# Kernel optimization log

Measured on AMD Instinct MI355X. Metric: run time of the kernel, lower is better.

## Reference

```python
import jax, jax.numpy as jnp
import numpy as np

# KroneckerLinear: W ~= sum_i (A_i kron B_i); efficient path computes, per token,
# Y = sum_i A_i @ X @ B_i^T with X = x.reshape(in1, in2), output flattened as (out1*out2).

IN1, IN2 = 64, 64      # in_factors (in1*in2 = in_features = 4096)
OUT1, OUT2 = 64, 64    # out_factors (out1*out2 = out_features = 4096)
NUM_SUM = 2
BATCH, SEQ = 4, 4096


def setup_inputs() -> dict:
    key = jax.random.key(0)
    kx, ka, kb, kbias = jax.random.split(key, 4)
    x = jax.random.normal(kx, (BATCH, SEQ, IN1 * IN2), dtype=jnp.float32)
    # kaiming-uniform-like scale for small factors
    bound_a = 1.0 / np.sqrt(IN1)
    bound_b = 1.0 / np.sqrt(IN2)
    A = jax.random.uniform(ka, (NUM_SUM, OUT1, IN1), dtype=jnp.float32, minval=-bound_a, maxval=bound_a)
    B = jax.random.uniform(kb, (NUM_SUM, OUT2, IN2), dtype=jnp.float32, minval=-bound_b, maxval=bound_b)
    bound = 1.0 / np.sqrt(IN1 * IN2)
    bias = jax.random.uniform(kbias, (OUT1 * OUT2,), dtype=jnp.float32, minval=-bound, maxval=bound)
    return {"x": x, "A": A, "B": B, "bias": bias}


def reference(x, A, B, bias):
    Bsz, T, _ = x.shape
    X = x.reshape(Bsz, T, IN1, IN2)  # (b, t, i, j)
    # y[b,t,o,p] = sum_s sum_ij A[s,o,i] * X[b,t,i,j] * B[s,p,j]  -> (out1, out2)
    y = jnp.einsum("btij,soi,spj->btop", X, A, B)
    return y.reshape(Bsz, T, OUT1 * OUT2) + bias
```

## Files before the change

kernel.cpp:

```cpp
#include <hip/hip_runtime.h>
#include <hip/hip_bf16.h>

typedef float  f32x4  __attribute__((ext_vector_type(4)));
typedef short  bf16x8 __attribute__((ext_vector_type(8)));

#define NT      16384
#define NBLOCK  256
#define WPB     4
#define NSTREAM (NBLOCK * WPB)
#define TPS     (NT / NSTREAM)

__device__ __forceinline__ short f2bf(float x) {
  return (short)__builtin_bit_cast(unsigned short, __float2bfloat16(x));
}

__device__ __forceinline__ void gload16(const float* gp, float* lp) {
  __builtin_amdgcn_global_load_lds((const __attribute__((address_space(1))) void*)gp,
                                   (__attribute__((address_space(3))) void*)lp,
                                   16, 0, 0);
}

__device__ __forceinline__ unsigned ldsaddr(const void* p) {
  return (unsigned)(uintptr_t)(const __attribute__((address_space(3))) void*)p;
}

__device__ __forceinline__ void stage(float* XB, const float* gbase, int lane) {
#pragma unroll
  for (int q = 0; q < 16; ++q) {
    const int i = q * 4 + (lane >> 4);
    const float* gp = gbase + i * 64 + (((lane & 15) ^ (i & 7)) << 2);
    gload16(gp, XB + q * 256);
  }
}

__global__ __launch_bounds__(256, 1)
void kron_kernel(const float* __restrict__ x,
                 const float* __restrict__ A,
                 const float* __restrict__ Bm,
                 const float* __restrict__ bias,
                 float* __restrict__ out) {
  __shared__ float  xh[WPB][2][4096];
  __shared__ bf16x8 AT[1024];
  __shared__ bf16x8 BT[1024];

  const int tid  = threadIdx.x;
  const int lane = tid & 63;
  const int w    = tid >> 6;
  const int g    = lane >> 4;
  const int l15  = lane & 15;
  const int sid  = blockIdx.x * WPB + w;

#pragma unroll
  for (int t = 0; t < 4; ++t) {
    const int idx = w * 4 + t;
    const int s = idx >> 3, ot = (idx & 7) >> 1, c = idx & 1;
    const int o = ot * 16 + l15;
    bf16x8 v;
#pragma unroll
    for (int e = 0; e < 8; ++e) {
      const int i = c * 32 + 4 * g + (e & 3) + 16 * (e >> 2);
      v[e] = f2bf(A[s * 4096 + o * 64 + i]);
    }
    AT[idx * 64 + lane] = v;
  }
#pragma unroll
  for (int t = 0; t < 4; ++t) {
    const int idx = w * 4 + t;
    const int s = idx >> 3, pt = (idx & 7) >> 1, jc = idx & 1;
    const int p = pt * 16 + l15;
    bf16x8 v;
#pragma unroll
    for (int e = 0; e < 8; ++e)
      v[e] = f2bf(Bm[s * 4096 + p * 64 + (jc * 32 + 8 * g + e)]);
    BT[idx * 64 + lane] = v;
  }

  const int pcol = 4 * g;
  f32x4 bv[4][4];
#pragma unroll
  for (int pt = 0; pt < 4; ++pt)
#pragma unroll
    for (int ot = 0; ot < 4; ++ot)
      bv[pt][ot] = *(const f32x4*)(bias + (ot * 16 + l15) * 64 + pt * 16 + pcol);

  __syncthreads();

  float* b0 = &xh[w][0][0];
  float* b1 = &xh[w][1][0];

  stage(b0, x + ((size_t)sid << 12), lane);
  stage(b1, x + ((size_t)(sid + NSTREAM) << 12), lane);

  for (int k = 0; k < TPS; ++k) {
    if (k == 0)                        asm volatile("s_waitcnt vmcnt(16)" ::: "memory");
    else if (k == 1 || k == TPS - 1)   asm volatile("s_waitcnt vmcnt(32)" ::: "memory");
    else                               asm volatile("s_waitcnt vmcnt(48)" ::: "memory");

    const unsigned ba = ldsaddr((k & 1) ? b1 : b0);
    f32x4 r0[4][2], r1[4][2];
#pragma unroll
    for (int it = 0; it < 4; ++it) {
      const unsigned base = ba + (unsigned)(it * 16 + l15) * 256u;
      const unsigned m    = (unsigned)(l15 & 7);
#pragma unroll
      for (int jc = 0; jc < 2; ++jc) {
        const unsigned c0 = (unsigned)(8 * jc + 2 * g);
        asm volatile("ds_read_b128 %0, %1" : "=v"(r0[it][jc]) : "v"(base + ((c0 ^ m) << 4)) : "memory");
        asm volatile("ds_read_b128 %0, %1" : "=v"(r1[it][jc]) : "v"(base + (((c0 + 1u) ^ m) << 4)) : "memory");
      }
    }
    asm volatile("s_waitcnt lgkmcnt(0)" ::: "memory");
    __builtin_amdgcn_sched_barrier(0);

    if (k + 2 < TPS)
      stage((k & 1) ? b1 : b0,
            x + ((size_t)((k + 2) * NSTREAM + sid) << 12), lane);

    bf16x8 xf[4][2];
#pragma unroll
    for (int it = 0; it < 4; ++it)
#pragma unroll
      for (int jc = 0; jc < 2; ++jc) {
        bf16x8 t;
        t[0]=f2bf(r0[it][jc][0]); t[1]=f2bf(r0[it][jc][1]);
        t[2]=f2bf(r0[it][jc][2]); t[3]=f2bf(r0[it][jc][3]);
        t[4]=f2bf(r1[it][jc][0]); t[5]=f2bf(r1[it][jc][1]);
        t[6]=f2bf(r1[it][jc][2]); t[7]=f2bf(r1[it][jc][3]);
        xf[it][jc] = t;
      }

    f32x4 acc2[4][4];
#pragma unroll
    for (int pt = 0; pt < 4; ++pt)
#pragma unroll
      for (int ot = 0; ot < 4; ++ot)
        acc2[pt][ot] = bv[pt][ot];

#pragma unroll
    for (int s = 0; s < 2; ++s) {
      bf16x8 bfr[4][2];
#pragma unroll
      for (int pt = 0; pt < 4; ++pt)
#pragma unroll
        for (int jc = 0; jc < 2; ++jc)
          bfr[pt][jc] = BT[(s * 8 + pt * 2 + jc) * 64 + lane];

      f32x4 a1[4][4];
#pragma unroll
      for (int a = 0; a < 4; ++a)
#pragma unroll
        for (int b = 0; b < 4; ++b)
          a1[a][b] = (f32x4){0.f, 0.f, 0.f, 0.f};
#pragma unroll
      for (int it = 0; it < 4; ++it)
#pragma unroll
        for (int pt = 0; pt < 4; ++pt)
#pragma unroll
          for (int jc = 0; jc < 2; ++jc)
            a1[it][pt] = __builtin_amdgcn_mfma_f32_16x16x32_bf16(
                xf[it][jc], bfr[pt][jc], a1[it][pt], 0, 0, 0);

      bf16x8 uf[4][2];
#pragma unroll
      for (int pt = 0; pt < 4; ++pt)
#pragma unroll
        for (int c = 0; c < 2; ++c) {
          bf16x8 t;
#pragma unroll
          for (int e = 0; e < 8; ++e)
            t[e] = f2bf(a1[(e >> 2) + 2 * c][pt][e & 3]);
          uf[pt][c] = t;
        }

      bf16x8 afr[4][2];
#pragma unroll
      for (int ot = 0; ot < 4; ++ot)
#pragma unroll
        for (int c = 0; c < 2; ++c)
          afr[ot][c] = AT[(s * 8 + ot * 2 + c) * 64 + lane];

#pragma unroll
      for (int pt = 0; pt < 4; ++pt)
#pragma unroll
        for (int ot = 0; ot < 4; ++ot)
#pragma unroll
          for (int c = 0; c < 2; ++c)
            acc2[pt][ot] = __builtin_amdgcn_mfma_f32_16x16x32_bf16(
                uf[pt][c], afr[ot][c], acc2[pt][ot], 0, 0, 0);
    }

    float* ob = out + (((size_t)(k * NSTREAM + sid)) << 12);
#pragma unroll
    for (int ot = 0; ot < 4; ++ot)
#pragma unroll
      for (int pt = 0; pt < 4; ++pt)
        *(f32x4*)(ob + (ot * 16 + l15) * 64 + pt * 16 + pcol) = acc2[pt][ot];
  }
}

extern "C" void kernel_launch(void* const* d_in, const int* in_sizes, int n_in,
                              void* d_out, int out_size, void* d_ws, size_t ws_size,
                              hipStream_t stream) {
  const float* x    = (const float*)d_in[0];
  const float* A    = (const float*)d_in[1];
  const float* B    = (const float*)d_in[2];
  const float* bias = (const float*)d_in[3];
  float* out        = (float*)d_out;
  kron_kernel<<<dim3(NBLOCK), dim3(256), 0, stream>>>(x, A, B, bias, out);
}
```

Before: 114.0 us.

## Split each token across four cooperating waves with LDS exchange of intermediates

Previously each wave processed its own whole token stream. Now a 256-thread block works on one token at a time, with each wave owning a 16-row slice of the first GEMM. The bf16 intermediate is exchanged through a swizzled LDS buffer so each wave can compute a 16-column slice of the output. This cuts register use per wave, allowing two blocks per CU and 512 blocks. The cost is added block-wide barriers per token and extra LDS traffic.

```diff
diff --git a/kernel.cpp b/kernel.cpp
--- a/kernel.cpp
+++ b/kernel.cpp
@@ -5,13 +5,14 @@
 typedef short  bf16x8 __attribute__((ext_vector_type(8)));
 
 #define NT      16384
-#define NBLOCK  256
-#define WPB     4
-#define NSTREAM (NBLOCK * WPB)
-#define TPS     (NT / NSTREAM)
+#define NBLOCK  512
+#define TPS     (NT / NBLOCK)
 
 __device__ __forceinline__ short f2bf(float x) {
   return (short)__builtin_bit_cast(unsigned short, __float2bfloat16(x));
+}
+__device__ __forceinline__ unsigned packbf2(float a, float b) {
+  return (unsigned)(unsigned short)f2bf(a) | ((unsigned)(unsigned short)f2bf(b) << 16);
 }
 
 __device__ __forceinline__ void gload16(const float* gp, float* lp) {
@@ -19,36 +20,37 @@
                                    (__attribute__((address_space(3))) void*)lp,
                                    16, 0, 0);
 }
-
 __device__ __forceinline__ unsigned ldsaddr(const void* p) {
   return (unsigned)(uintptr_t)(const __attribute__((address_space(3))) void*)p;
 }
 
-__device__ __forceinline__ void stage(float* XB, const float* gbase, int lane) {
+__device__ __forceinline__ void stageQW(float* XB, const float* gbase, int w, int lane) {
 #pragma unroll
-  for (int q = 0; q < 16; ++q) {
+  for (int qq = 0; qq < 4; ++qq) {
+    const int q = w * 4 + qq;
     const int i = q * 4 + (lane >> 4);
     const float* gp = gbase + i * 64 + (((lane & 15) ^ (i & 7)) << 2);
     gload16(gp, XB + q * 256);
   }
 }
 
-__global__ __launch_bounds__(256, 1)
+__global__ __launch_bounds__(256, 2)
 void kron_kernel(const float* __restrict__ x,
                  const float* __restrict__ A,
                  const float* __restrict__ Bm,
                  const float* __restrict__ bias,
                  float* __restrict__ out) {
-  __shared__ float  xh[WPB][2][4096];
+  __shared__ float  xb[2][4096];
   __shared__ bf16x8 AT[1024];
   __shared__ bf16x8 BT[1024];
+  __shared__ unsigned long long Ul[2048];
 
   const int tid  = threadIdx.x;
   const int lane = tid & 63;
   const int w    = tid >> 6;
   const int g    = lane >> 4;
   const int l15  = lane & 15;
-  const int sid  = blockIdx.x * WPB + w;
+  const int blk  = blockIdx.x;
 
 #pragma unroll
   for (int t = 0; t < 4; ++t) {
@@ -75,126 +77,94 @@
     BT[idx * 64 + lane] = v;
   }
 
-  const int pcol = 4 * g;
-  f32x4 bv[4][4];
+  f32x4 bv[4];
 #pragma unroll
-  for (int pt = 0; pt < 4; ++pt)
-#pragma unroll
-    for (int ot = 0; ot < 4; ++ot)
-      bv[pt][ot] = *(const f32x4*)(bias + (ot * 16 + l15) * 64 + pt * 16 + pcol);
+  for (int ot = 0; ot < 4; ++ot)
+    bv[ot] = *(const f32x4*)(bias + (ot * 16 + l15) * 64 + w * 16 + 4 * g);
 
   __syncthreads();
 
-  float* b0 = &xh[w][0][0];
-  float* b1 = &xh[w][1][0];
+  stageQW(&xb[0][0], x + ((size_t)blk << 12), w, lane);
+  stageQW(&xb[1][0], x + ((size_t)(blk + NBLOCK) << 12), w, lane);
+  asm volatile("s_waitcnt vmcnt(4)" ::: "memory");
+  __builtin_amdgcn_s_barrier();
 
-  stage(b0, x + ((size_t)sid << 12), lane);
-  stage(b1, x + ((size_t)(sid + NSTREAM) << 12), lane);
+  const unsigned wsw = (unsigned)(2 * ((l15 >> 2) & 1));
 
   for (int k = 0; k < TPS; ++k) {
-    if (k == 0)                        asm volatile("s_waitcnt vmcnt(16)" ::: "memory");
-    else if (k == 1 || k == TPS - 1)   asm volatile("s_waitcnt vmcnt(32)" ::: "memory");
-    else                               asm volatile("s_waitcnt vmcnt(48)" ::: "memory");
-
-    const unsigned ba = ldsaddr((k & 1) ? b1 : b0);
-    f32x4 r0[4][2], r1[4][2];
+    const unsigned ba   = ldsaddr(&xb[k & 1][0]);
+    const unsigned base = ba + (unsigned)(w * 16 + l15) * 256u;
+    const unsigned m    = (unsigned)(l15 & 7);
+    f32x4 r0[2], r1[2];
 #pragma unroll
-    for (int it = 0; it < 4; ++it) {
-      const unsigned base = ba + (unsigned)(it * 16 + l15) * 256u;
-      const unsigned m    = (unsigned)(l15 & 7);
-#pragma unroll
-      for (int jc = 0; jc < 2; ++jc) {
-        const unsigned c0 = (unsigned)(8 * jc + 2 * g);
-        asm volatile("ds_read_b128 %0, %1" : "=v"(r0[it][jc]) : "v"(base + ((c0 ^ m) << 4)) : "memory");
-        asm volatile("ds_read_b128 %0, %1" : "=v"(r1[it][jc]) : "v"(base + (((c0 + 1u) ^ m) << 4)) : "memory");
-      }
+    for (int jc = 0; jc < 2; ++jc) {
+      const unsigned c0 = (unsigned)(8 * jc + 2 * g);
+      asm volatile("ds_read_b128 %0, %1" : "=v"(r0[jc]) : "v"(base + ((c0 ^ m) << 4)) : "memory");
+      asm volatile("ds_read_b128 %0, %1" : "=v"(r1[jc]) : "v"(base + (((c0 + 1u) ^ m) << 4)) : "memory");
     }
     asm volatile("s_waitcnt lgkmcnt(0)" ::: "memory");
     __builtin_amdgcn_sched_barrier(0);
 
-    if (k + 2 < TPS)
-      stage((k & 1) ? b1 : b0,
-            x + ((size_t)((k + 2) * NSTREAM + sid) << 12), lane);
-
-    bf16x8 xf[4][2];
+    bf16x8 xf[2];
 #pragma unroll
-    for (int it = 0; it < 4; ++it)
-#pragma unroll
-      for (int jc = 0; jc < 2; ++jc) {
-        bf16x8 t;
-        t[0]=f2bf(r0[it][jc][0]); t[1]=f2bf(r0[it][jc][1]);
-        t[2]=f2bf(r0[it][jc][2]); t[3]=f2bf(r0[it][jc][3]);
-        t[4]=f2bf(r1[it][jc][0]); t[5]=f2bf(r1[it][jc][1]);
-        t[6]=f2bf(r1[it][jc][2]); t[7]=f2bf(r1[it][jc][3]);
-        xf[it][jc] = t;
-      }
-
-    f32x4 acc2[4][4];
-#pragma unroll
-    for (int pt = 0; pt < 4; ++pt)
-#pragma unroll
-      for (int ot = 0; ot < 4; ++ot)
-        acc2[pt][ot] = bv[pt][ot];
+    for (int jc = 0; jc < 2; ++jc) {
+      bf16x8 t;
+      t[0]=f2bf(r0[jc][0]); t[1]=f2bf(r0[jc][1]); t[2]=f2bf(r0[jc][2]); t[3]=f2bf(r0[jc][3]);
+      t[4]=f2bf(r1[jc][0]); t[5]=f2bf(r1[jc][1]); t[6]=f2bf(r1[jc][2]); t[7]=f2bf(r1[jc][3]);
+      xf[jc] = t;
+    }
 
 #pragma unroll
     for (int s = 0; s < 2; ++s) {
-      bf16x8 bfr[4][2];
 #pragma unroll
-      for (int pt = 0; pt < 4; ++pt)
+      for (int pt = 0; pt < 4; ++pt) {
+        f32x4 a1 = (f32x4){0.f, 0.f, 0.f, 0.f};
 #pragma unroll
         for (int jc = 0; jc < 2; ++jc)
-          bfr[pt][jc] = BT[(s * 8 + pt * 2 + jc) * 64 + lane];
+          a1 = __builtin_amdgcn_mfma_f32_16x16x32_bf16(
+              xf[jc], BT[(s * 8 + pt * 2 + jc) * 64 + lane], a1, 0, 0, 0);
+        const unsigned lo = packbf2(a1[0], a1[1]);
+        const unsigned hi = packbf2(a1[2], a1[3]);
+        Ul[((((s * 4 + pt) * 4 + g) * 16 + l15) << 2) + ((unsigned)w ^ wsw)] =
+            ((unsigned long long)hi << 32) | lo;
+      }
+    }
 
-      f32x4 a1[4][4];
+    asm volatile("s_waitcnt lgkmcnt(0)" ::: "memory");
+    __builtin_amdgcn_sched_barrier(0);
+    __builtin_amdgcn_s_barrier();
+
+    if (k + 2 < TPS)
+      stageQW(&xb[k & 1][0], x + ((size_t)(blk + (k + 2) * NBLOCK) << 12), w, lane);
+
+    f32x4 acc[4];
 #pragma unroll
-      for (int a = 0; a < 4; ++a)
+    for (int ot = 0; ot < 4; ++ot) acc[ot] = bv[ot];
 #pragma unroll
-        for (int b = 0; b < 4; ++b)
-          a1[a][b] = (f32x4){0.f, 0.f, 0.f, 0.f};
+    for (int s = 0; s < 2; ++s) {
+      bf16x8 uf[2];
 #pragma unroll
-      for (int it = 0; it < 4; ++it)
-#pragma unroll
-        for (int pt = 0; pt < 4; ++pt)
-#pragma unroll
-          for (int jc = 0; jc < 2; ++jc)
-            a1[it][pt] = __builtin_amdgcn_mfma_f32_16x16x32_bf16(
-                xf[it][jc], bfr[pt][jc], a1[it][pt], 0, 0, 0);
-
-      bf16x8 uf[4][2];
-#pragma unroll
-      for (int pt = 0; pt < 4; ++pt)
-#pragma unroll
-        for (int c = 0; c < 2; ++c) {
-          bf16x8 t;
-#pragma unroll
-          for (int e = 0; e < 8; ++e)
-            t[e] = f2bf(a1[(e >> 2) + 2 * c][pt][e & 3]);
-          uf[pt][c] = t;
-        }
-
-      bf16x8 afr[4][2];
+      for (int c = 0; c < 2; ++c) {
+        const unsigned q2 = (unsigned)((l15 >> 2) & 1);
+        uf[c] = *reinterpret_cast<const bf16x8*>(
+            &Ul[((((s * 4 + w) * 4 + g) * 16 + l15) << 2) + 2u * ((unsigned)c ^ q2)]);
+      }
 #pragma unroll
       for (int ot = 0; ot < 4; ++ot)
 #pragma unroll
         for (int c = 0; c < 2; ++c)
-          afr[ot][c] = AT[(s * 8 + ot * 2 + c) * 64 + lane];
-
-#pragma unroll
-      for (int pt = 0; pt < 4; ++pt)
-#pragma unroll
-        for (int ot = 0; ot < 4; ++ot)
-#pragma unroll
-          for (int c = 0; c < 2; ++c)
-            acc2[pt][ot] = __builtin_amdgcn_mfma_f32_16x16x32_bf16(
-                uf[pt][c], afr[ot][c], acc2[pt][ot], 0, 0, 0);
+          acc[ot] = __builtin_amdgcn_mfma_f32_16x16x32_bf16(
+              uf[c], AT[(s * 8 + ot * 2 + c) * 64 + lane], acc[ot], 0, 0, 0);
     }
 
-    float* ob = out + (((size_t)(k * NSTREAM + sid)) << 12);
+    float* ob = out + ((size_t)(blk + k * NBLOCK) << 12);
 #pragma unroll
     for (int ot = 0; ot < 4; ++ot)
-#pragma unroll
-      for (int pt = 0; pt < 4; ++pt)
-        *(f32x4*)(ob + (ot * 16 + l15) * 64 + pt * 16 + pcol) = acc2[pt][ot];
+      *(f32x4*)(ob + (ot * 16 + l15) * 64 + w * 16 + 4 * g) = acc[ot];
+
+    asm volatile("s_waitcnt vmcnt(8) lgkmcnt(0)" ::: "memory");
+    __builtin_amdgcn_sched_barrier(0);
+    __builtin_amdgcn_s_barrier();
   }
 }
 
```

Result: faster. 105.3 us (-7.6%).
